# Performance work log

Hardware: AMD Instinct MI355X
Metric: run time of the kernel (lower is better)

Reference implementation:

```python
import jax, jax.numpy as jnp
import numpy as np

NEG_INF = -1.0e9
KQ_DIM = 64


def setup_inputs() -> dict:
    key = jax.random.key(0)
    ks = jax.random.split(key, 10)
    S, B, H, DK, DV = 2048, 8, 512, 64, 64
    q = jax.random.normal(ks[0], (S, B, H), dtype=jnp.float32)
    k = jax.random.normal(ks[1], (S, B, H), dtype=jnp.float32)
    v = jax.random.normal(ks[2], (S, B, H), dtype=jnp.float32)
    attn_mask = jax.random.bernoulli(ks[3], 0.1, (S, B))          # (q_seq, batch)
    key_padding_mask = jax.random.bernoulli(ks[4], 0.1, (B, S))   # (batch, k_seq)
    scale = 0.02
    Wq = jax.random.normal(ks[5], (DK, H), dtype=jnp.float32) * scale
    bq = jnp.zeros((DK,), dtype=jnp.float32)
    Wk = jax.random.normal(ks[6], (DK, H), dtype=jnp.float32) * scale
    bk = jnp.zeros((DK,), dtype=jnp.float32)
    Wv = jax.random.normal(ks[7], (DV, H), dtype=jnp.float32) * scale
    bv = jnp.zeros((DV,), dtype=jnp.float32)
    return {
        "q_hidden_inputs": q, "k_hidden_inputs": k, "v_hidden_inputs": v,
        "Wq": Wq, "bq": bq, "Wk": Wk, "bk": bk, "Wv": Wv, "bv": bv,
        "attn_mask": attn_mask, "key_padding_mask": key_padding_mask,
    }


def reference(q_hidden_inputs, k_hidden_inputs, v_hidden_inputs,
              Wq, bq, Wk, bk, Wv, bv, attn_mask, key_padding_mask):
    # inputs are (seq, batch, hidden) -> (batch, seq, hidden)
    q = jnp.transpose(q_hidden_inputs, (1, 0, 2))
    k = jnp.transpose(k_hidden_inputs, (1, 0, 2))
    v = jnp.transpose(v_hidden_inputs, (1, 0, 2))
    # pre-projection key padding mask: fill padded key hidden states with -1e9
    k = jnp.where(key_padding_mask[:, :, None], NEG_INF, k)
    queries = jnp.einsum('bsh,dh->bsd', q, Wq) + bq   # (B, Sq, DK)
    keys = jnp.einsum('bsh,dh->bsd', k, Wk) + bk      # (B, Sk, DK)
    values = jnp.einsum('bsh,dh->bsd', v, Wv) + bv    # (B, Sk, DV)
    scores = jnp.einsum('bqd,bkd->bqk', queries, keys) / jnp.sqrt(jnp.float32(KQ_DIM))
    # attn_mask (Sq, B) -> (B, Sq, 1): masks whole query rows, broadcast over keys
    scores = jnp.where(jnp.transpose(attn_mask, (1, 0))[:, :, None], NEG_INF, scores)
    probs = jax.nn.softmax(scores, axis=-1)           # (B, Sq, Sk)
    out = jnp.einsum('bqk,bkd->bqd', probs, values)   # (B, Sq, DV)
    return jnp.transpose(out, (1, 0, 2))              # (Sq, B, DV)
```

## Files before the change

kernel.cpp:

```cpp
#include <hip/hip_runtime.h>
#include <stdint.h>

#define S_LEN 2048
#define BATCH 8
#define HID   512
#define DD    64

typedef __bf16 bf16x8 __attribute__((ext_vector_type(8)));
typedef float  f32x4  __attribute__((ext_vector_type(4)));

#define WS_QB 0
#define WS_KB (2*1024*1024)
#define WS_VB (4*1024*1024)
#define WS_VT (6*1024*1024)
#define WS_MS (8*1024*1024)
#define WS_U  (WS_MS + 65536)
#define WS_C  (WS_U + 2048)
#define WS_KM (WS_C + 16)
#define WS_FLP (WS_KM + 256)
#define WS_CTP (WS_FLP + 256)
#define WS_DT (WS_CTP + 256)
#define WS_AM (WS_DT + 16)
#define WS_KP (WS_AM + 16384)
#define WS_PT (9*1024*1024)
#define PT_BYTES(ks) ((size_t)(ks) * 8 * 2048 * 68 * 4)

__device__ inline unsigned short f2bf(float f) {
    union { float f; unsigned u; } v; v.f = f;
    unsigned r = v.u + 0x7FFFu + ((v.u >> 16) & 1u);
    return (unsigned short)(r >> 16);
}

__device__ inline unsigned short f2bfc(float f) {
    __bf16 h = (__bf16)f;
    return __builtin_bit_cast(unsigned short, h);
}

__device__ inline bf16x8 load8(const unsigned short* p) {
    uint4 t = *(const uint4*)p;
    return __builtin_bit_cast(bf16x8, t);
}

__global__ void kA_detect(const float* __restrict__ Wk, const float* __restrict__ bk,
                          const void* am_raw, const void* kpm_raw,
                          int* __restrict__ gflp, float* __restrict__ kmask)
{
    int bi = blockIdx.x, tid = threadIdx.x;
    if (bi < 32) {
        __shared__ int smask[2];
        if (tid < 2) smask[tid] = 0;
        __syncthreads();
        for (int mi = 0; mi < 2; ++mi) {
            const unsigned char* base = (const unsigned char*)(mi ? kpm_raw : am_raw);
            const unsigned char*      p8  = base + bi * 512;
            const unsigned short*     p16 = (const unsigned short*)base + bi * 256;
            const unsigned int*       p32 = (const unsigned int*)base + bi * 128;
            const unsigned long long* p64 = (const unsigned long long*)base + bi * 64;
            int v[8] = {0,0,0,0,0,0,0,0};
            if (tid < 64) {
                unsigned long long w = p64[tid];
                if (w != 0ull && w != 0x3FF0000000000000ull) v[0] = 1;
                if (w > 1ull)                                v[1] = 1;
            }
            if (tid < 128) {
                unsigned w = p32[tid];
                if (w != 0u && w != 0x3F800000u) v[2] = 1;
                if (w > 1u)                      v[3] = 1;
            }
            {
                unsigned short w = p16[tid];
                if (w != 0 && w != 0x3F80) v[4] = 1;
                if (w != 0 && w != 0x3C00) v[5] = 1;
                if (w > 1)                 v[6] = 1;
            }
            if (p8[tid] > 1 || p8[tid + 256] > 1) v[7] = 1;
            int bits = 0;
            #pragma unroll
            for (int j = 0; j < 8; ++j)
                if (v[j]) bits |= (1 << j);
            if (bits) atomicOr(&smask[mi], bits);
        }
        __syncthreads();
        if (tid < 2) gflp[bi * 2 + tid] = smask[tid];
    } else {
        __shared__ float r[256];
        int d = bi - 32;
        const float* wr = Wk + (size_t)d * HID;
        r[tid] = wr[tid] + wr[tid + 256];
        __syncthreads();
        for (int off = 128; off > 0; off >>= 1) {
            if (tid < off) r[tid] += r[tid + off];
            __syncthreads();
        }
        if (tid == 0) kmask[d] = -1.0e9f * r[0] + bk[d];
    }
}

__global__ void kB_finish(const void* am_raw, const void* kpm_raw,
                          const int* __restrict__ gflp,
                          const float* __restrict__ Wq, const float* __restrict__ bq,
                          const float* __restrict__ kmask,
                          unsigned char* __restrict__ am8,
                          unsigned char* __restrict__ kp8,
                          int* __restrict__ cntp, int* __restrict__ dts,
                          float* __restrict__ u, float* __restrict__ cbuf)
{
    int bi = blockIdx.x, tid = threadIdx.x;
    if (bi < 32) {
        int m[2] = {0, 0};
        #pragma unroll 8
        for (int i = 0; i < 32; ++i) { m[0] |= gflp[i * 2]; m[1] |= gflp[i * 2 + 1]; }
        __shared__ int scnt[2];
        if (tid < 2) scnt[tid] = 0;
        __syncthreads();
        for (int mi = 0; mi < 2; ++mi) {
            int d = 8;
            #pragma unroll
            for (int j = 7; j >= 0; --j)
                if (!((m[mi] >> j) & 1)) d = j;
            const unsigned char*      p8  = (const unsigned char*)(mi ? kpm_raw : am_raw);
            const unsigned short*     p16 = (const unsigned short*)p8;
            const unsigned int*       p32 = (const unsigned int*)p8;
            const unsigned long long* p64 = (const unsigned long long*)p8;
            unsigned char* dst = mi ? kp8 : am8;
            int c = 0;
            #pragma unroll
            for (int it = 0; it < 2; ++it) {
                int e = bi * 512 + tid + it * 256;
                int bbit;
                if (d <= 1)      bbit = (p64[e] != 0ull);
                else if (d <= 3) bbit = (p32[e] != 0u);
                else if (d <= 6) bbit = (p16[e] != 0);
                else             bbit = (p8[e]  != 0);
                dst[e] = (unsigned char)bbit;
                c += bbit;
            }
            c += __shfl_xor(c, 1);  c += __shfl_xor(c, 2);
            c += __shfl_xor(c, 4);  c += __shfl_xor(c, 8);
            c += __shfl_xor(c, 16); c += __shfl_xor(c, 32);
            if ((tid & 63) == 0) atomicAdd(&scnt[mi], c);
            if (bi == 0 && tid == 0) dts[mi] = d;
        }
        __syncthreads();
        if (tid < 2) cntp[bi * 2 + tid] = scnt[tid];
    } else if (bi == 32) {
        __shared__ float kml[64];
        if (tid < 64) kml[tid] = kmask[tid];
        __syncthreads();
        for (int h = tid; h < HID; h += 256) {
            float s = 0.f;
            #pragma unroll 8
            for (int d = 0; d < 64; ++d) s += Wq[(size_t)d * HID + h] * kml[d];
            u[h] = s;
        }
    } else {
        __shared__ float ca[64];
        if (tid < 64) ca[tid] = bq[tid] * kmask[tid];
        __syncthreads();
        if (tid == 0) {
            float s = 0.f;
            #pragma unroll
            for (int d = 0; d < 64; ++d) s += ca[d];
            *cbuf = s;
        }
    }
}

__launch_bounds__(256)
__global__ void k1_proj(const float* __restrict__ q, const float* __restrict__ k,
                        const float* __restrict__ v,
                        const float* __restrict__ Wq, const float* __restrict__ bq,
                        const float* __restrict__ Wk, const float* __restrict__ bk,
                        const float* __restrict__ Wv, const float* __restrict__ bv,
                        unsigned short* __restrict__ Qb, unsigned short* __restrict__ Kb,
                        unsigned short* __restrict__ Vb,
                        const float* __restrict__ u, const float* __restrict__ cbuf,
                        float* __restrict__ msc)
{
    __shared__ __align__(16) unsigned short la[64][72];
    __shared__ __align__(16) unsigned short lw[64][72];
    __shared__ float msum[64][4];

    const float *X, *W, *bias; unsigned short* Y; int do_ms;
    if (blockIdx.y == 0)      { X = q; W = Wq; bias = bq; Y = Qb; do_ms = 1; }
    else if (blockIdx.y == 1) { X = k; W = Wk; bias = bk; Y = Kb; do_ms = 0; }
    else                      { X = v; W = Wv; bias = bv; Y = Vb; do_ms = 0; }

    int tid = threadIdx.x;
    int w = tid >> 6, lane = tid & 63;
    int g = lane >> 4, r16 = lane & 15;
    int r0 = blockIdx.x * 64;
    int srow = tid >> 2, sq = tid & 3;

    float mac = 0.f;
    f32x4 acc[4];
    #pragma unroll
    for (int i = 0; i < 4; ++i) acc[i] = (f32x4){0.f, 0.f, 0.f, 0.f};

    for (int k0 = 0; k0 < HID; k0 += 64) {
        __syncthreads();
        {
            const float* xr = X + (size_t)(r0 + srow) * HID + k0 + sq * 16;
            float xv[16];
            #pragma unroll
            for (int i = 0; i < 16; i += 4) {
                float4 t = *(const float4*)(xr + i);
                xv[i] = t.x; xv[i+1] = t.y; xv[i+2] = t.z; xv[i+3] = t.w;
            }
            if (do_ms) {
                const float* ur = u + k0 + sq * 16;
                #pragma unroll
                for (int i = 0; i < 16; ++i) mac += xv[i] * ur[i];
            }
            unsigned short hx[16] __attribute__((aligned(16)));
            #pragma unroll
            for (int i = 0; i < 16; ++i) hx[i] = f2bfc(xv[i]);
            *(uint4*)&la[srow][sq * 16]     = *(uint4*)hx;
            *(uint4*)&la[srow][sq * 16 + 8] = *(uint4*)(hx + 8);

            const float* wr = W + (size_t)srow * HID + k0 + sq * 16;
            float wv[16];
            #pragma unroll
            for (int i = 0; i < 16; i += 4) {
                float4 t = *(const float4*)(wr + i);
                wv[i] = t.x; wv[i+1] = t.y; wv[i+2] = t.z; wv[i+3] = t.w;
            }
            unsigned short hw[16] __attribute__((aligned(16)));
            #pragma unroll
            for (int i = 0; i < 16; ++i) hw[i] = f2bfc(wv[i]);
            *(uint4*)&lw[srow][sq * 16]     = *(uint4*)hw;
            *(uint4*)&lw[srow][sq * 16 + 8] = *(uint4*)(hw + 8);
        }
        __syncthreads();
        #pragma unroll
        for (int h = 0; h < 2; ++h) {
            bf16x8 af = load8(&la[w * 16 + r16][h * 32 + g * 8]);
            #pragma unroll
            for (int d4 = 0; d4 < 4; ++d4) {
                bf16x8 bf = load8(&lw[d4 * 16 + r16][h * 32 + g * 8]);
                acc[d4] = __builtin_amdgcn_mfma_f32_16x16x32_bf16(af, bf, acc[d4], 0, 0, 0);
            }
        }
    }

    if (do_ms) msum[srow][sq] = mac;
    __syncthreads();

    float bv4[4];
    #pragma unroll
    for (int d4 = 0; d4 < 4; ++d4) bv4[d4] = bias[d4 * 16 + r16];
    #pragma unroll
    for (int d4 = 0; d4 < 4; ++d4) {
        #pragma unroll
        for (int vv = 0; vv < 4; ++vv) {
            int r = r0 + w * 16 + 4 * g + vv;
            int bb = r & 7, ss = r >> 3;
            Y[((size_t)bb * S_LEN + ss) * DD + d4 * 16 + r16] = f2bfc(acc[d4][vv] + bv4[d4]);
        }
    }
    if (do_ms && tid < 64) {
        int r = r0 + tid;
        float m = (msum[tid][0] + msum[tid][1] + msum[tid][2] + msum[tid][3] + *cbuf) * 0.125f;
        msc[(size_t)(r & 7) * S_LEN + (r >> 3)] = m;
    }
}

__launch_bounds__(256)
__global__ void kT_transpose(const unsigned short* __restrict__ Vb,
                             unsigned short* __restrict__ Vt)
{
    __shared__ __align__(16) unsigned short t[64][72];
    int b = blockIdx.y, s0 = blockIdx.x * 64;
    int tid = threadIdx.x;
    int skey = tid & 63, sdq = (tid >> 6) * 16;
    {
        const unsigned short* vp = Vb + ((size_t)b * S_LEN + s0 + skey) * DD + sdq;
        uint4 t0 = *(const uint4*)vp;
        uint4 t1 = *(const uint4*)(vp + 8);
        unsigned short tmp[16];
        *(uint4*)tmp = t0; *(uint4*)(tmp + 8) = t1;
        #pragma unroll
        for (int i = 0; i < 16; ++i) t[sdq + i][skey] = tmp[i];
    }
    __syncthreads();
    int dv = tid >> 2, kseg = (tid & 3) * 16;
    unsigned short* dst = Vt + (((size_t)b * 32 + (s0 >> 6)) * 64 + dv) * 64 + kseg;
    uint4 a0 = *(const uint4*)&t[dv][kseg];
    uint4 a1 = *(const uint4*)&t[dv][kseg + 8];
    *(uint4*)dst       = a0;
    *(uint4*)(dst + 8) = a1;
}

__launch_bounds__(256)
__global__ void k2_attn(const unsigned short* __restrict__ Qb,
                        const unsigned short* __restrict__ Kb,
                        const unsigned short* __restrict__ Vt,
                        const float* __restrict__ msc,
                        const unsigned char* __restrict__ am8,
                        const unsigned char* __restrict__ kp8,
                        float* __restrict__ part, int ks)
{
    __shared__ __align__(16) unsigned short kl[64][72];
    __shared__ __align__(16) unsigned short vl[64][72];
    __shared__ __align__(16) unsigned short pl[4][16][72];

    int tid = threadIdx.x;
    int w = tid >> 6, lane = tid & 63;
    int g = lane >> 4, r16 = lane & 15;
    int b = blockIdx.y;
    int z = blockIdx.z;
    int q0 = blockIdx.x * 64 + w * 16;
    int kspan = S_LEN / ks;
    int kbeg = z * kspan;
    int nt = kspan >> 6;

    int srow = tid >> 2, sseg = (tid & 3) * 16;
    const unsigned short* kstage = Kb + ((size_t)b * S_LEN + srow) * DD + sseg;
    const unsigned short* vstage = Vt + (size_t)b * (32 * 64 * 64) + srow * 64 + sseg;

    const unsigned short* qp = Qb + ((size_t)b * S_LEN + q0 + r16) * DD + g * 8;
    bf16x8 qa0 = load8(qp);
    bf16x8 qa1 = load8(qp + 32);

    int qq = q0 + r16;
    float mscv = msc[(size_t)b * S_LEN + qq];
    int qm = am8[qq * 8 + b];
    const unsigned char* kpb = kp8 + (size_t)b * S_LEN + 4 * g;

    float mrun = -1.0e30f, lsum = 0.f;
    f32x4 acco[4];
    #pragma unroll
    for (int i = 0; i < 4; ++i) acco[i] = (f32x4){0.f, 0.f, 0.f, 0.f};

    for (int t = 0; t < nt; ++t) {
        int kt0 = kbeg + t * 64;
        __syncthreads();
        {
            const unsigned short* kp = kstage + (size_t)kt0 * DD;
            uint4 a0 = *(const uint4*)kp;
            uint4 a1 = *(const uint4*)(kp + 8);
            *(uint4*)&kl[srow][sseg]     = a0;
            *(uint4*)&kl[srow][sseg + 8] = a1;
        }
        {
            const unsigned short* vp = vstage + (size_t)(kt0 >> 6) * 4096;
            uint4 a0 = *(const uint4*)vp;
            uint4 a1 = *(const uint4*)(vp + 8);
            *(uint4*)&vl[srow][sseg]     = a0;
            *(uint4*)&vl[srow][sseg + 8] = a1;
        }
        __syncthreads();

        f32x4 accs[4];
        #pragma unroll
        for (int kt = 0; kt < 4; ++kt) {
            accs[kt] = (f32x4){0.f, 0.f, 0.f, 0.f};
            bf16x8 kb0 = load8(&kl[kt * 16 + r16][g * 8]);
            bf16x8 kb1 = load8(&kl[kt * 16 + r16][32 + g * 8]);
            accs[kt] = __builtin_amdgcn_mfma_f32_16x16x32_bf16(kb0, qa0, accs[kt], 0, 0, 0);
            accs[kt] = __builtin_amdgcn_mfma_f32_16x16x32_bf16(kb1, qa1, accs[kt], 0, 0, 0);
        }

        float p[4][4];
        #pragma unroll
        for (int kt = 0; kt < 4; ++kt) {
            unsigned kp4 = *(const unsigned*)(kpb + kt0 + kt * 16);
            #pragma unroll
            for (int vv = 0; vv < 4; ++vv) {
                float s = accs[kt][vv] * 0.125f;
                if ((kp4 >> (8 * vv)) & 0xFFu) s = mscv;
                if (qm) s = -1.0e9f;
                p[kt][vv] = s;
            }
        }

        float mt = p[0][0];
        #pragma unroll
        for (int kt = 0; kt < 4; ++kt)
            #pragma unroll
            for (int vv = 0; vv < 4; ++vv)
                mt = fmaxf(mt, p[kt][vv]);
        mt = fmaxf(mt, __shfl_xor(mt, 16));
        mt = fmaxf(mt, __shfl_xor(mt, 32));

        float mn = fmaxf(mrun, mt);
        float f = __expf(mrun - mn);
        mrun = mn;

        float ps = 0.f;
        #pragma unroll
        for (int kt = 0; kt < 4; ++kt)
            #pragma unroll
            for (int vv = 0; vv < 4; ++vv) {
                float pv = __expf(p[kt][vv] - mn);
                p[kt][vv] = pv;
                ps += pv;
            }
        ps += __shfl_xor(ps, 16);
        ps += __shfl_xor(ps, 32);
        lsum = lsum * f + ps;
        #pragma unroll
        for (int d4 = 0; d4 < 4; ++d4) acco[d4] *= f;

        #pragma unroll
        for (int kt = 0; kt < 4; ++kt) {
            unsigned w0 = (unsigned)f2bf(p[kt][0]) | ((unsigned)f2bf(p[kt][1]) << 16);
            unsigned w1 = (unsigned)f2bf(p[kt][2]) | ((unsigned)f2bf(p[kt][3]) << 16);
            unsigned short* dst = &pl[w][r16][kt * 16 + 4 * g];
            *(unsigned*)dst       = w0;
            *(unsigned*)(dst + 2) = w1;
        }

        #pragma unroll
        for (int h = 0; h < 2; ++h) {
            bf16x8 pa = load8(&pl[w][r16][h * 32 + g * 8]);
            #pragma unroll
            for (int d4 = 0; d4 < 4; ++d4) {
                bf16x8 vb = load8(&vl[d4 * 16 + r16][h * 32 + g * 8]);
                acco[d4] = __builtin_amdgcn_mfma_f32_16x16x32_bf16(vb, pa, acco[d4], 0, 0, 0);
            }
        }
    }

    float* pp = part + ((size_t)(z * BATCH + b) * S_LEN + qq) * 68;
    #pragma unroll
    for (int d4 = 0; d4 < 4; ++d4)
        *(float4*)(pp + d4 * 16 + 4 * g) =
            make_float4(acco[d4][0], acco[d4][1], acco[d4][2], acco[d4][3]);
    if (g == 0) { pp[64] = mrun; pp[65] = lsum; }
}

__global__ void k2c_combine(const float* __restrict__ part, float* __restrict__ out, int ks)
{
    int t = blockIdx.x * 64 + threadIdx.x;
    int row = t >> 2, seg = t & 3;
    int b = row >> 11, qq = row & 2047;

    float M = -3.0e38f;
    #pragma unroll
    for (int z = 0; z < 8; ++z)
        if (z < ks)
            M = fmaxf(M, part[((size_t)(z * BATCH + b) * S_LEN + qq) * 68 + 64]);

    float lt = 0.f;
    float4 r0 = make_float4(0.f,0.f,0.f,0.f), r1 = r0, r2 = r0, r3 = r0;
    #pragma unroll
    for (int z = 0; z < 8; ++z) {
        if (z < ks) {
            const float* pp = part + ((size_t)(z * BATCH + b) * S_LEN + qq) * 68;
            float wv = __expf(pp[64] - M);
            lt += pp[65] * wv;
            const float* ps = pp + seg * 16;
            float4 a0 = *(const float4*)(ps);
            float4 a1 = *(const float4*)(ps + 4);
            float4 a2 = *(const float4*)(ps + 8);
            float4 a3 = *(const float4*)(ps + 12);
            r0.x += a0.x*wv; r0.y += a0.y*wv; r0.z += a0.z*wv; r0.w += a0.w*wv;
            r1.x += a1.x*wv; r1.y += a1.y*wv; r1.z += a1.z*wv; r1.w += a1.w*wv;
            r2.x += a2.x*wv; r2.y += a2.y*wv; r2.z += a2.z*wv; r2.w += a2.w*wv;
            r3.x += a3.x*wv; r3.y += a3.y*wv; r3.z += a3.z*wv; r3.w += a3.w*wv;
        }
    }
    float inv = 1.f / lt;
    float* op = out + ((size_t)qq * BATCH + b) * DD + seg * 16;
    *(float4*)(op)      = make_float4(r0.x*inv, r0.y*inv, r0.z*inv, r0.w*inv);
    *(float4*)(op + 4)  = make_float4(r1.x*inv, r1.y*inv, r1.z*inv, r1.w*inv);
    *(float4*)(op + 8)  = make_float4(r2.x*inv, r2.y*inv, r2.z*inv, r2.w*inv);
    *(float4*)(op + 12) = make_float4(r3.x*inv, r3.y*inv, r3.z*inv, r3.w*inv);
}

__global__ void k3_diag(const int* __restrict__ cntp, const int* __restrict__ dts,
                        float* __restrict__ out, int bad_sizes)
{
    int c0 = 0, c1 = 0;
    #pragma unroll 8
    for (int i = 0; i < 32; ++i) { c0 += cntp[i * 2]; c1 += cntp[i * 2 + 1]; }
    float dg = 0.f;
    if (bad_sizes)                   dg = 1.0e6f;
    else if (c0 < 164 || c0 > 8192)  dg = 2.0e6f + (float)dts[0] * 1.0e5f;
    else if (c1 < 164 || c1 > 8192)  dg = 6.0e6f + (float)dts[1] * 1.0e5f;
    if (dg != 0.f) out[0] = dg;
}

extern "C" void kernel_launch(void* const* d_in, const int* in_sizes, int n_in,
                              void* d_out, int out_size, void* d_ws, size_t ws_size,
                              hipStream_t stream) {
    const float* q   = (const float*)d_in[0];
    const float* k   = (const float*)d_in[1];
    const float* v   = (const float*)d_in[2];
    const float* Wq  = (const float*)d_in[3];
    const float* bq  = (const float*)d_in[4];
    const float* Wk  = (const float*)d_in[5];
    const float* bk  = (const float*)d_in[6];
    const float* Wv  = (const float*)d_in[7];
    const float* bv  = (const float*)d_in[8];
    const void*  am  = d_in[9];
    const void*  kpm = d_in[10];

    char* ws = (char*)d_ws;
    unsigned short* Qb = (unsigned short*)(ws + WS_QB);
    unsigned short* Kb = (unsigned short*)(ws + WS_KB);
    unsigned short* Vb = (unsigned short*)(ws + WS_VB);
    unsigned short* Vt = (unsigned short*)(ws + WS_VT);
    float* msc = (float*)(ws + WS_MS);
    float* u   = (float*)(ws + WS_U);
    float* cb  = (float*)(ws + WS_C);
    float* km  = (float*)(ws + WS_KM);
    int*  gflp = (int*)(ws + WS_FLP);
    int*  cntp = (int*)(ws + WS_CTP);
    int*   dts = (int*)(ws + WS_DT);
    unsigned char* am8 = (unsigned char*)(ws + WS_AM);
    unsigned char* kp8 = (unsigned char*)(ws + WS_KP);
    float* part = (float*)(ws + WS_PT);

    int ok = (n_in == 11)
        && in_sizes[0] == 8388608 && in_sizes[1] == 8388608 && in_sizes[2] == 8388608
        && in_sizes[3] == 32768 && in_sizes[4] == 64
        && in_sizes[5] == 32768 && in_sizes[6] == 64
        && in_sizes[7] == 32768 && in_sizes[8] == 64
        && in_sizes[9] == 16384 && in_sizes[10] == 16384
        && out_size == 1048576;

    int ks = 1;
    if      (ws_size >= (size_t)WS_PT + PT_BYTES(8)) ks = 8;
    else if (ws_size >= (size_t)WS_PT + PT_BYTES(4)) ks = 4;
    else if (ws_size >= (size_t)WS_PT + PT_BYTES(2)) ks = 2;

    kA_detect<<<96, 256, 0, stream>>>(Wk, bk, am, kpm, gflp, km);
    kB_finish<<<34, 256, 0, stream>>>(am, kpm, gflp, Wq, bq, km,
                                      am8, kp8, cntp, dts, u, cb);

    dim3 g1(256, 3);
    k1_proj<<<g1, 256, 0, stream>>>(q, k, v, Wq, bq, Wk, bk, Wv, bv,
                                    Qb, Kb, Vb, u, cb, msc);

    dim3 gt(32, 8);
    kT_transpose<<<gt, 256, 0, stream>>>(Vb, Vt);

    dim3 g2(32, 8, ks);
    k2_attn<<<g2, 256, 0, stream>>>(Qb, Kb, Vt, msc, am8, kp8, part, ks);

    k2c_combine<<<1024, 64, 0, stream>>>(part, (float*)d_out, ks);

    k3_diag<<<1, 1, 0, stream>>>(cntp, dts, (float*)d_out, !ok);
}
```

Baseline: 80.41 us.

## Load projection A-fragments directly, prefetch K/V tiles, widen combine kernel

The projection kernel now loads each wave's X rows straight from global memory into MFMA A-fragments, dropping the shared-memory staging tile and the msum reduction in favour of wave shuffles. The attention kernel register-prefetches the next K and V tile while computing on the current one, overlapping global loads with MFMA work. The combine kernel uses 16 threads per row with one float4 each and 256-thread blocks for more parallelism. Direct X loads from each lane are less coalesced, and prefetching raises register pressure.

```diff
diff --git a/kernel.cpp b/kernel.cpp
--- a/kernel.cpp
+++ b/kernel.cpp
@@ -41,6 +41,13 @@
     return __builtin_bit_cast(bf16x8, t);
 }
 
+__device__ inline bf16x8 pack8(float4 a, float4 b) {
+    unsigned short h[8] __attribute__((aligned(16)));
+    h[0]=f2bfc(a.x); h[1]=f2bfc(a.y); h[2]=f2bfc(a.z); h[3]=f2bfc(a.w);
+    h[4]=f2bfc(b.x); h[5]=f2bfc(b.y); h[6]=f2bfc(b.z); h[7]=f2bfc(b.w);
+    return load8(h);
+}
+
 __global__ void kA_detect(const float* __restrict__ Wk, const float* __restrict__ bk,
                           const void* am_raw, const void* kpm_raw,
                           int* __restrict__ gflp, float* __restrict__ kmask)
@@ -177,9 +184,7 @@
                         const float* __restrict__ u, const float* __restrict__ cbuf,
                         float* __restrict__ msc)
 {
-    __shared__ __align__(16) unsigned short la[64][72];
     __shared__ __align__(16) unsigned short lw[64][72];
-    __shared__ float msum[64][4];
 
     const float *X, *W, *bias; unsigned short* Y; int do_ms;
     if (blockIdx.y == 0)      { X = q; W = Wq; bias = bq; Y = Qb; do_ms = 1; }
@@ -192,6 +197,8 @@
     int r0 = blockIdx.x * 64;
     int srow = tid >> 2, sq = tid & 3;
 
+    const float* xrow = X + (size_t)(r0 + w * 16 + r16) * HID;
+
     float mac = 0.f;
     f32x4 acc[4];
     #pragma unroll
@@ -200,24 +207,6 @@
     for (int k0 = 0; k0 < HID; k0 += 64) {
         __syncthreads();
         {
-            const float* xr = X + (size_t)(r0 + srow) * HID + k0 + sq * 16;
-            float xv[16];
-            #pragma unroll
-            for (int i = 0; i < 16; i += 4) {
-                float4 t = *(const float4*)(xr + i);
-                xv[i] = t.x; xv[i+1] = t.y; xv[i+2] = t.z; xv[i+3] = t.w;
-            }
-            if (do_ms) {
-                const float* ur = u + k0 + sq * 16;
-                #pragma unroll
-                for (int i = 0; i < 16; ++i) mac += xv[i] * ur[i];
-            }
-            unsigned short hx[16] __attribute__((aligned(16)));
-            #pragma unroll
-            for (int i = 0; i < 16; ++i) hx[i] = f2bfc(xv[i]);
-            *(uint4*)&la[srow][sq * 16]     = *(uint4*)hx;
-            *(uint4*)&la[srow][sq * 16 + 8] = *(uint4*)(hx + 8);
-
             const float* wr = W + (size_t)srow * HID + k0 + sq * 16;
             float wv[16];
             #pragma unroll
@@ -231,20 +220,31 @@
             *(uint4*)&lw[srow][sq * 16]     = *(uint4*)hw;
             *(uint4*)&lw[srow][sq * 16 + 8] = *(uint4*)(hw + 8);
         }
-        __syncthreads();
-        #pragma unroll
-        for (int h = 0; h < 2; ++h) {
-            bf16x8 af = load8(&la[w * 16 + r16][h * 32 + g * 8]);
-            #pragma unroll
-            for (int d4 = 0; d4 < 4; ++d4) {
-                bf16x8 bf = load8(&lw[d4 * 16 + r16][h * 32 + g * 8]);
-                acc[d4] = __builtin_amdgcn_mfma_f32_16x16x32_bf16(af, bf, acc[d4], 0, 0, 0);
-            }
-        }
-    }
-
-    if (do_ms) msum[srow][sq] = mac;
-    __syncthreads();
+        float4 xa = *(const float4*)(xrow + k0 + g * 8);
+        float4 xb = *(const float4*)(xrow + k0 + g * 8 + 4);
+        float4 xc = *(const float4*)(xrow + k0 + 32 + g * 8);
+        float4 xd = *(const float4*)(xrow + k0 + 32 + g * 8 + 4);
+        if (do_ms) {
+            float4 ua = *(const float4*)(u + k0 + g * 8);
+            float4 ub = *(const float4*)(u + k0 + g * 8 + 4);
+            float4 uc = *(const float4*)(u + k0 + 32 + g * 8);
+            float4 ud = *(const float4*)(u + k0 + 32 + g * 8 + 4);
+            mac += xa.x*ua.x + xa.y*ua.y + xa.z*ua.z + xa.w*ua.w;
+            mac += xb.x*ub.x + xb.y*ub.y + xb.z*ub.z + xb.w*ub.w;
+            mac += xc.x*uc.x + xc.y*uc.y + xc.z*uc.z + xc.w*uc.w;
+            mac += xd.x*ud.x + xd.y*ud.y + xd.z*ud.z + xd.w*ud.w;
+        }
+        bf16x8 af0 = pack8(xa, xb);
+        bf16x8 af1 = pack8(xc, xd);
+        __syncthreads();
+        #pragma unroll
+        for (int d4 = 0; d4 < 4; ++d4) {
+            bf16x8 bf0 = load8(&lw[d4 * 16 + r16][g * 8]);
+            acc[d4] = __builtin_amdgcn_mfma_f32_16x16x32_bf16(af0, bf0, acc[d4], 0, 0, 0);
+            bf16x8 bf1 = load8(&lw[d4 * 16 + r16][32 + g * 8]);
+            acc[d4] = __builtin_amdgcn_mfma_f32_16x16x32_bf16(af1, bf1, acc[d4], 0, 0, 0);
+        }
+    }
 
     float bv4[4];
     #pragma unroll
@@ -258,10 +258,13 @@
             Y[((size_t)bb * S_LEN + ss) * DD + d4 * 16 + r16] = f2bfc(acc[d4][vv] + bv4[d4]);
         }
     }
-    if (do_ms && tid < 64) {
-        int r = r0 + tid;
-        float m = (msum[tid][0] + msum[tid][1] + msum[tid][2] + msum[tid][3] + *cbuf) * 0.125f;
-        msc[(size_t)(r & 7) * S_LEN + (r >> 3)] = m;
+    if (do_ms) {
+        mac += __shfl_xor(mac, 16);
+        mac += __shfl_xor(mac, 32);
+        if (g == 0) {
+            int r = r0 + w * 16 + r16;
+            msc[(size_t)(r & 7) * S_LEN + (r >> 3)] = (mac + *cbuf) * 0.125f;
+        }
     }
 }
 
@@ -332,24 +335,27 @@
     #pragma unroll
     for (int i = 0; i < 4; ++i) acco[i] = (f32x4){0.f, 0.f, 0.f, 0.f};
 
+    uint4 ka0 = *(const uint4*)(kstage + (size_t)kbeg * DD);
+    uint4 ka1 = *(const uint4*)(kstage + (size_t)kbeg * DD + 8);
+    uint4 va0 = *(const uint4*)(vstage + (size_t)(kbeg >> 6) * 4096);
+    uint4 va1 = *(const uint4*)(vstage + (size_t)(kbeg >> 6) * 4096 + 8);
+
     for (int t = 0; t < nt; ++t) {
         int kt0 = kbeg + t * 64;
         __syncthreads();
-        {
-            const unsigned short* kp = kstage + (size_t)kt0 * DD;
-            uint4 a0 = *(const uint4*)kp;
-            uint4 a1 = *(const uint4*)(kp + 8);
-            *(uint4*)&kl[srow][sseg]     = a0;
-            *(uint4*)&kl[srow][sseg + 8] = a1;
-        }
-        {
-            const unsigned short* vp = vstage + (size_t)(kt0 >> 6) * 4096;
-            uint4 a0 = *(const uint4*)vp;
-            uint4 a1 = *(const uint4*)(vp + 8);
-            *(uint4*)&vl[srow][sseg]     = a0;
-            *(uint4*)&vl[srow][sseg + 8] = a1;
-        }
-        __syncthreads();
+        *(uint4*)&kl[srow][sseg]     = ka0;
+        *(uint4*)&kl[srow][sseg + 8] = ka1;
+        *(uint4*)&vl[srow][sseg]     = va0;
+        *(uint4*)&vl[srow][sseg + 8] = va1;
+        __syncthreads();
+
+        if (t + 1 < nt) {
+            int kn = kt0 + 64;
+            ka0 = *(const uint4*)(kstage + (size_t)kn * DD);
+            ka1 = *(const uint4*)(kstage + (size_t)kn * DD + 8);
+            va0 = *(const uint4*)(vstage + (size_t)(kn >> 6) * 4096);
+            va1 = *(const uint4*)(vstage + (size_t)(kn >> 6) * 4096 + 8);
+        }
 
         f32x4 accs[4];
         #pragma unroll
@@ -432,8 +438,8 @@
 
 __global__ void k2c_combine(const float* __restrict__ part, float* __restrict__ out, int ks)
 {
-    int t = blockIdx.x * 64 + threadIdx.x;
-    int row = t >> 2, seg = t & 3;
+    int t = blockIdx.x * 256 + threadIdx.x;
+    int row = t >> 4, s16 = t & 15;
     int b = row >> 11, qq = row & 2047;
 
     float M = -3.0e38f;
@@ -443,30 +449,20 @@
             M = fmaxf(M, part[((size_t)(z * BATCH + b) * S_LEN + qq) * 68 + 64]);
 
     float lt = 0.f;
-    float4 r0 = make_float4(0.f,0.f,0.f,0.f), r1 = r0, r2 = r0, r3 = r0;
+    float4 r = make_float4(0.f, 0.f, 0.f, 0.f);
     #pragma unroll
     for (int z = 0; z < 8; ++z) {
         if (z < ks) {
             const float* pp = part + ((size_t)(z * BATCH + b) * S_LEN + qq) * 68;
             float wv = __expf(pp[64] - M);
             lt += pp[65] * wv;
-            const float* ps = pp + seg * 16;
-            float4 a0 = *(const float4*)(ps);
-            float4 a1 = *(const float4*)(ps + 4);
-            float4 a2 = *(const float4*)(ps + 8);
-            float4 a3 = *(const float4*)(ps + 12);
-            r0.x += a0.x*wv; r0.y += a0.y*wv; r0.z += a0.z*wv; r0.w += a0.w*wv;
-            r1.x += a1.x*wv; r1.y += a1.y*wv; r1.z += a1.z*wv; r1.w += a1.w*wv;
-            r2.x += a2.x*wv; r2.y += a2.y*wv; r2.z += a2.z*wv; r2.w += a2.w*wv;
-            r3.x += a3.x*wv; r3.y += a3.y*wv; r3.z += a3.z*wv; r3.w += a3.w*wv;
+            float4 a = *(const float4*)(pp + s16 * 4);
+            r.x += a.x * wv; r.y += a.y * wv; r.z += a.z * wv; r.w += a.w * wv;
         }
     }
     float inv = 1.f / lt;
-    float* op = out + ((size_t)qq * BATCH + b) * DD + seg * 16;
-    *(float4*)(op)      = make_float4(r0.x*inv, r0.y*inv, r0.z*inv, r0.w*inv);
-    *(float4*)(op + 4)  = make_float4(r1.x*inv, r1.y*inv, r1.z*inv, r1.w*inv);
-    *(float4*)(op + 8)  = make_float4(r2.x*inv, r2.y*inv, r2.z*inv, r2.w*inv);
-    *(float4*)(op + 12) = make_float4(r3.x*inv, r3.y*inv, r3.z*inv, r3.w*inv);
+    float* op = out + ((size_t)qq * BATCH + b) * DD + s16 * 4;
+    *(float4*)op = make_float4(r.x * inv, r.y * inv, r.z * inv, r.w * inv);
 }
 
 __global__ void k3_diag(const int* __restrict__ cntp, const int* __restrict__ dts,
@@ -540,7 +536,7 @@
     dim3 g2(32, 8, ks);
     k2_attn<<<g2, 256, 0, stream>>>(Qb, Kb, Vt, msc, am8, kp8, part, ks);
 
-    k2c_combine<<<1024, 64, 0, stream>>>(part, (float*)d_out, ks);
+    k2c_combine<<<1024, 256, 0, stream>>>(part, (float*)d_out, ks);
 
     k3_diag<<<1, 1, 0, stream>>>(cntp, dts, (float*)d_out, !ok);
 }
```

Measured after the change: 78.16 us. 1.03x faster.
